# Optimization experiments

Measured on AMD Instinct MI355X. Metric: run time of the kernel, lower is better.

## Reference

```python
import jax, jax.numpy as jnp
import numpy as np

B, T, P, E = 4, 16, 256, 768
H, D = 12, 64          # num_heads, kq_size; H*D == E
DFF = 3072
SCALE = D ** (-0.5)
EPS = 1e-5


def _ln(x, g, b):
    m = jnp.mean(x, axis=-1, keepdims=True)
    v = jnp.mean((x - m) ** 2, axis=-1, keepdims=True)
    return (x - m) / jnp.sqrt(v + EPS) * g + b


def setup_inputs() -> dict:
    key = jax.random.key(0)
    ks = jax.random.split(key, 16)
    std = 0.02
    d = {"x": jax.random.normal(ks[0], (B, T, P, E), jnp.float32)}
    # spatial attention params (weights stored as (in, out))
    d["sq_w"] = jax.random.normal(ks[1], (E, H * D), jnp.float32) * std
    d["sk_w"] = jax.random.normal(ks[2], (E, H * D), jnp.float32) * std
    d["sv_w"] = jax.random.normal(ks[3], (E, H * D), jnp.float32) * std
    d["so_w"] = jax.random.normal(ks[4], (H * D, E), jnp.float32) * std
    d["sq_b"] = jnp.zeros((H * D,), jnp.float32)
    d["sk_b"] = jnp.zeros((H * D,), jnp.float32)
    d["sv_b"] = jnp.zeros((H * D,), jnp.float32)
    d["so_b"] = jnp.zeros((E,), jnp.float32)
    d["sg"] = jnp.ones((E,), jnp.float32)
    d["sb"] = jnp.zeros((E,), jnp.float32)
    # temporal attention params
    d["tq_w"] = jax.random.normal(ks[5], (E, H * D), jnp.float32) * std
    d["tk_w"] = jax.random.normal(ks[6], (E, H * D), jnp.float32) * std
    d["tv_w"] = jax.random.normal(ks[7], (E, H * D), jnp.float32) * std
    d["to_w"] = jax.random.normal(ks[8], (H * D, E), jnp.float32) * std
    d["tq_b"] = jnp.zeros((H * D,), jnp.float32)
    d["tk_b"] = jnp.zeros((H * D,), jnp.float32)
    d["tv_b"] = jnp.zeros((H * D,), jnp.float32)
    d["to_b"] = jnp.zeros((E,), jnp.float32)
    d["tg"] = jnp.ones((E,), jnp.float32)
    d["tb"] = jnp.zeros((E,), jnp.float32)
    # FFN + final layernorm
    d["w1"] = jax.random.normal(ks[9], (E, DFF), jnp.float32) * std
    d["b1"] = jnp.zeros((DFF,), jnp.float32)
    d["w2"] = jax.random.normal(ks[10], (DFF, E), jnp.float32) * std
    d["b2"] = jnp.zeros((E,), jnp.float32)
    d["g"] = jnp.ones((E,), jnp.float32)
    d["bb"] = jnp.zeros((E,), jnp.float32)
    return d


def reference(x, sq_w, sq_b, sk_w, sk_b, sv_w, sv_b, so_w, so_b, sg, sb,
              tq_w, tq_b, tk_w, tk_b, tv_w, tv_b, to_w, to_b, tg, tb,
              w1, b1, w2, b2, g, bb):
    b, t, p, e = x.shape

    # ---- Spatial layer: attention over patches P within each frame ----
    q = (x @ sq_w + sq_b).reshape(b, t, p, H, D)
    k = (x @ sk_w + sk_b).reshape(b, t, p, H, D)
    v = (x @ sv_w + sv_b).reshape(b, t, p, H, D)
    attn = jnp.einsum('btphd,btqhd->bthpq', q, k) * SCALE
    attn = jax.nn.softmax(attn, axis=-1)
    out = jnp.einsum('bthpq,btqhd->btphd', attn, v).reshape(b, t, p, H * D)
    out = out @ so_w + so_b
    x = _ln(x + out, sg, sb)

    # ---- Temporal layer: causal attention over frames T per patch ----
    q = (x @ tq_w + tq_b).reshape(b, t, p, H, D)
    k = (x @ tk_w + tk_b).reshape(b, t, p, H, D)
    v = (x @ tv_w + tv_b).reshape(b, t, p, H, D)
    attn = jnp.einsum('btphd,bsphd->bphts', q, k) * SCALE
    causal = jnp.where(jnp.arange(t)[:, None] >= jnp.arange(t)[None, :],
                       jnp.float32(0), -jnp.inf).astype(x.dtype)  # (T, T)
    attn = attn + causal
    attn = jax.nn.softmax(attn, axis=-1)
    out = jnp.einsum('bphts,bsphd->btphd', attn, v).reshape(b, t, p, H * D)
    out = out @ to_w + to_b
    x = _ln(x + out, tg, tb)

    # ---- Feed forward + final layernorm ----
    ff = jax.nn.gelu(x @ w1 + b1, approximate=False) @ w2 + b2
    x = _ln(x + ff, g, bb)
    return x
```

## Files before the change

### kernel.cpp

```cpp
#include <hip/hip_runtime.h>
#include <math.h>

constexpr int cB   = 4;
constexpr int cT   = 16;
constexpr int cP   = 256;
constexpr int cE   = 768;
constexpr int cH   = 12;
constexpr int cD   = 64;
constexpr int cDFF = 3072;
constexpr int NTOK = cB * cT * cP;
constexpr float cSCALE = 0.125f;
constexpr float cEPS = 1e-5f;

typedef __attribute__((ext_vector_type(8))) short short8;
typedef __attribute__((ext_vector_type(4))) float f32x4;
typedef __attribute__((ext_vector_type(8))) unsigned short u16x8;
typedef __attribute__((ext_vector_type(4))) unsigned short u16x4;

#define AS1 __attribute__((address_space(1)))
#define AS3 __attribute__((address_space(3)))

__device__ inline float b2f(unsigned short u) {
    union { unsigned int i; float f; } c; c.i = ((unsigned int)u) << 16; return c.f;
}
__device__ inline unsigned short f2b(float f) {
    union { float f; unsigned int i; } c; c.f = f;
    unsigned int i = c.i;
    unsigned int r = i + 0x7FFFu + ((i >> 16) & 1u);
    return (unsigned short)(r >> 16);
}

__device__ inline void gload16(const unsigned short* g, short* l) {
    __builtin_amdgcn_global_load_lds((AS1 const void*)g, (AS3 void*)l, 16, 0, 0);
}

template<int OUTB, int ACT, int SPLIT3>
__global__ __launch_bounds__(512, 1) void gemm256_kernel(
    const unsigned short* __restrict__ A,
    const unsigned short* __restrict__ BT,
    const float* __restrict__ bias0, const float* __restrict__ bias1,
    const float* __restrict__ bias2,
    void* __restrict__ C0, void* __restrict__ C1, void* __restrict__ C2,
    int M, int N, int K, int nbn)
{
    __shared__ short LDS[3 * 24576];

    const int tid = threadIdx.x;
    const int w = tid >> 6, l = tid & 63;
    const int l15 = l & 15, l16 = l >> 4;
    const int wm = w >> 1, wn = w & 1;
    const int srow = l >> 3;
    const int sslot = l & 7;

    const int nwg = gridDim.x;
    const int wg = (blockIdx.x & 7) * (nwg >> 3) + (blockIdx.x >> 3);
    const int bm = wg / nbn, bn = wg % nbn;
    const int m0 = bm * 256, n0 = bn * 128;

    f32x4 acc[4][4];
    #pragma unroll
    for (int i = 0; i < 4; ++i)
        #pragma unroll
        for (int j = 0; j < 4; ++j)
            #pragma unroll
            for (int r = 0; r < 4; ++r) acc[i][j][r] = 0.f;

    const int nt = K >> 6;

    const unsigned short* gA[4];
    const unsigned short* gB[2];
    int dA[4], dB[2];
    #pragma unroll
    for (int j = 0; j < 4; ++j) {
        const int r = w * 32 + j * 8 + srow;
        gA[j] = A + (size_t)(m0 + r) * K + ((sslot ^ (r & 7)) << 3);
        dA[j] = r * 64 + (sslot << 3);
    }
    #pragma unroll
    for (int j = 0; j < 2; ++j) {
        const int r = w * 8 + j * 64 + srow;
        gB[j] = BT + (size_t)(n0 + r) * K + ((sslot ^ (r & 7)) << 3);
        dB[j] = 16384 + r * 64 + (sslot << 3);
    }

    int offA[4][2], offB[4][2];
    #pragma unroll
    for (int mm = 0; mm < 4; ++mm) {
        const int ra = wm * 64 + mm * 16 + l15;
        const int sw = (ra & 7) << 4;
        offA[mm][0] = ra * 128 + ((l16 * 16) ^ sw);
        offA[mm][1] = ra * 128 + ((64 + l16 * 16) ^ sw);
    }
    #pragma unroll
    for (int nf = 0; nf < 4; ++nf) {
        const int rb = wn * 64 + nf * 16 + l15;
        const int sw = (rb & 7) << 4;
        offB[nf][0] = 32768 + rb * 128 + ((l16 * 16) ^ sw);
        offB[nf][1] = 32768 + rb * 128 + ((64 + l16 * 16) ^ sw);
    }

    #pragma unroll
    for (int j = 0; j < 4; ++j) { gload16(gA[j], LDS + dA[j]); }
    #pragma unroll
    for (int j = 0; j < 2; ++j) { gload16(gB[j], LDS + dB[j]); }
    #pragma unroll
    for (int j = 0; j < 4; ++j) { gload16(gA[j] + 64, LDS + 24576 + dA[j]); }
    #pragma unroll
    for (int j = 0; j < 2; ++j) { gload16(gB[j] + 64, LDS + 24576 + dB[j]); }
    #pragma unroll
    for (int j = 0; j < 4; ++j) gA[j] += 128;
    #pragma unroll
    for (int j = 0; j < 2; ++j) gB[j] += 128;

    asm volatile("s_waitcnt vmcnt(6)" ::: "memory");
    __builtin_amdgcn_s_barrier();

    int buf = 0;
    for (int t = 0; t < nt; ++t) {
        const char* Lb = (const char*)LDS + buf * 49152;

        short8 aF[4][2], bF[4][2];
        #pragma unroll
        for (int mm = 0; mm < 4; ++mm)
            aF[mm][0] = *(const short8*)(Lb + offA[mm][0]);
        #pragma unroll
        for (int nf = 0; nf < 4; ++nf)
            bF[nf][0] = *(const short8*)(Lb + offB[nf][0]);
        __builtin_amdgcn_sched_barrier(0);
        #pragma unroll
        for (int mm = 0; mm < 4; ++mm)
            aF[mm][1] = *(const short8*)(Lb + offA[mm][1]);
        #pragma unroll
        for (int nf = 0; nf < 4; ++nf)
            bF[nf][1] = *(const short8*)(Lb + offB[nf][1]);

        if (t + 2 < nt) {
            const int b2 = (buf == 0) ? 2 : buf - 1;
            short* dst = LDS + b2 * 24576;
            #pragma unroll
            for (int j = 0; j < 4; ++j) { gload16(gA[j], dst + dA[j]); gA[j] += 64; }
            #pragma unroll
            for (int j = 0; j < 2; ++j) { gload16(gB[j], dst + dB[j]); gB[j] += 64; }
        }

        asm volatile("s_waitcnt lgkmcnt(8)" ::: "memory");
        __builtin_amdgcn_sched_barrier(0);
        __builtin_amdgcn_s_setprio(1);
        #pragma unroll
        for (int nf = 0; nf < 4; ++nf)
            #pragma unroll
            for (int mm = 0; mm < 4; ++mm)
                acc[mm][nf] = __builtin_amdgcn_mfma_f32_16x16x32_bf16(
                    aF[mm][0], bF[nf][0], acc[mm][nf], 0, 0, 0);
        __builtin_amdgcn_s_setprio(0);
        asm volatile("s_waitcnt lgkmcnt(0)" ::: "memory");
        __builtin_amdgcn_sched_barrier(0);
        __builtin_amdgcn_s_setprio(1);
        #pragma unroll
        for (int nf = 0; nf < 4; ++nf)
            #pragma unroll
            for (int mm = 0; mm < 4; ++mm)
                acc[mm][nf] = __builtin_amdgcn_mfma_f32_16x16x32_bf16(
                    aF[mm][1], bF[nf][1], acc[mm][nf], 0, 0, 0);
        __builtin_amdgcn_s_setprio(0);

        if (t + 1 < nt) {
            if (t + 2 < nt)
                asm volatile("s_waitcnt vmcnt(6)" ::: "memory");
            else
                asm volatile("s_waitcnt vmcnt(0)" ::: "memory");
            __builtin_amdgcn_s_barrier();
        }
        buf = (buf == 2) ? 0 : buf + 1;
    }

    #pragma unroll
    for (int mf = 0; mf < 4; ++mf) {
        #pragma unroll
        for (int nf = 0; nf < 4; ++nf) {
            const int ng = n0 + wn * 64 + nf * 16 + l15;
            int nl = ng;
            const float* bp = bias0;
            void* Cp = C0;
            int Nout = N;
            if (SPLIT3) {
                const int which = ng / 768;
                nl = ng - which * 768;
                bp = (which == 0) ? bias0 : (which == 1) ? bias1 : bias2;
                Cp = (which == 0) ? C0 : (which == 1) ? C1 : C2;
                Nout = 768;
            }
            const float bs = bp[nl];
            #pragma unroll
            for (int r = 0; r < 4; ++r) {
                const int row = m0 + wm * 64 + mf * 16 + l16 * 4 + r;
                float v = acc[mf][nf][r] + bs;
                if (ACT) v = 0.5f * v * (1.f + erff(v * 0.70710678118654752f));
                if (OUTB) ((unsigned short*)Cp)[(size_t)row * Nout + nl] = f2b(v);
                else      ((float*)Cp)[(size_t)row * Nout + nl] = v;
            }
        }
    }
}

template<int OUTB, int ACT>
__global__ __launch_bounds__(256) void gemm128_kernel(
    const unsigned short* __restrict__ A,
    const unsigned short* __restrict__ BT,
    const float* __restrict__ bias,
    void* __restrict__ Cout,
    int M, int N, int K)
{
    __shared__ short As[8192];
    __shared__ short Bs[8192];

    const int tid = threadIdx.x;
    const int m0 = blockIdx.y * 128;
    const int n0 = blockIdx.x * 128;
    const int w  = tid >> 6;
    const int l  = tid & 63;
    const int wr = w >> 1, wc = w & 1;
    const int l15 = l & 15, l16 = l >> 4;

    f32x4 acc[4][4];
    #pragma unroll
    for (int i = 0; i < 4; ++i)
        #pragma unroll
        for (int j = 0; j < 4; ++j)
            #pragma unroll
            for (int r = 0; r < 4; ++r) acc[i][j][r] = 0.f;

    const int sr = tid >> 2;
    const int sc = (tid & 3) << 3;
    const unsigned short* ga0 = A  + (size_t)(m0 + sr) * K + sc;
    const unsigned short* ga1 = A  + (size_t)(m0 + 64 + sr) * K + sc;
    const unsigned short* gb0 = BT + (size_t)(n0 + sr) * K + sc;
    const unsigned short* gb1 = BT + (size_t)(n0 + 64 + sr) * K + sc;
    short* lA = As + tid * 8;
    short* lB = Bs + tid * 8;

    const int aoff = (wr * 64 + l15) * 32 + l16 * 8;
    const int boff = (wc * 64 + l15) * 32 + l16 * 8;

    gload16(ga0, lA);
    gload16(ga1, lA + 2048);
    gload16(gb0, lB);
    gload16(gb1, lB + 2048);
    __syncthreads();

    int cur = 0;
    for (int k0 = 0; k0 < K; k0 += 32) {
        if (k0 + 32 < K) {
            const int nb = (cur ^ 1) << 12;
            gload16(ga0 + k0 + 32, lA + nb);
            gload16(ga1 + k0 + 32, lA + nb + 2048);
            gload16(gb0 + k0 + 32, lB + nb);
            gload16(gb1 + k0 + 32, lB + nb + 2048);
        }
        const int cb = cur << 12;
        short8 aF[4], bF[4];
        #pragma unroll
        for (int mf = 0; mf < 4; ++mf)
            aF[mf] = *(const short8*)(As + cb + aoff + mf * 512);
        #pragma unroll
        for (int nf = 0; nf < 4; ++nf)
            bF[nf] = *(const short8*)(Bs + cb + boff + nf * 512);
        #pragma unroll
        for (int mf = 0; mf < 4; ++mf)
            #pragma unroll
            for (int nf = 0; nf < 4; ++nf)
                acc[mf][nf] = __builtin_amdgcn_mfma_f32_16x16x32_bf16(
                    aF[mf], bF[nf], acc[mf][nf], 0, 0, 0);
        __syncthreads();
        cur ^= 1;
    }

    #pragma unroll
    for (int mf = 0; mf < 4; ++mf) {
        #pragma unroll
        for (int nf = 0; nf < 4; ++nf) {
            const int col = n0 + wc * 64 + nf * 16 + l15;
            const float bs = bias[col];
            #pragma unroll
            for (int r = 0; r < 4; ++r) {
                const int row = m0 + wr * 64 + mf * 16 + l16 * 4 + r;
                float v = acc[mf][nf][r] + bs;
                if (ACT) v = 0.5f * v * (1.f + erff(v * 0.70710678118654752f));
                if (OUTB) ((unsigned short*)Cout)[(size_t)row * N + col] = f2b(v);
                else      ((float*)Cout)[(size_t)row * N + col] = v;
            }
        }
    }
}

__global__ __launch_bounds__(256) void transpose_cast_kernel(
    const float* __restrict__ W, unsigned short* __restrict__ WT,
    int K, int N)
{
    __shared__ float t[32][33];
    const int k0 = blockIdx.y * 32;
    const int n0 = blockIdx.x * 32;
    const int tx = threadIdx.x & 31;
    const int ty4 = (threadIdx.x >> 5) << 2;
    #pragma unroll
    for (int i = 0; i < 4; ++i)
        t[ty4 + i][tx] = W[(size_t)(k0 + ty4 + i) * N + n0 + tx];
    __syncthreads();
    #pragma unroll
    for (int i = 0; i < 4; ++i)
        WT[(size_t)(n0 + ty4 + i) * K + k0 + tx] = f2b(t[tx][ty4 + i]);
}

struct TP8 { const float* src[8]; unsigned short* dst[8]; };
__global__ __launch_bounds__(256) void transpose_cast8_kernel(TP8 p)
{
    __shared__ float t[32][33];
    const int z = blockIdx.z;
    const float* W = p.src[z];
    unsigned short* WT = p.dst[z];
    const int k0 = blockIdx.y * 32;
    const int n0 = blockIdx.x * 32;
    const int tx = threadIdx.x & 31;
    const int ty4 = (threadIdx.x >> 5) << 2;
    #pragma unroll
    for (int i = 0; i < 4; ++i)
        t[ty4 + i][tx] = W[(size_t)(k0 + ty4 + i) * cE + n0 + tx];
    __syncthreads();
    #pragma unroll
    for (int i = 0; i < 4; ++i)
        WT[(size_t)(n0 + ty4 + i) * cE + k0 + tx] = f2b(t[tx][ty4 + i]);
}

__global__ __launch_bounds__(256) void cast_bf16_kernel(
    const float* __restrict__ in, unsigned short* __restrict__ out, int n4)
{
    for (int i = blockIdx.x * blockDim.x + threadIdx.x; i < n4;
         i += gridDim.x * blockDim.x) {
        float4 v = ((const float4*)in)[i];
        u16x4 o;
        o[0] = f2b(v.x); o[1] = f2b(v.y); o[2] = f2b(v.z); o[3] = f2b(v.w);
        *(u16x4*)(out + (size_t)i * 4) = o;
    }
}

__global__ __launch_bounds__(256) void residual_ln_kernel(
    const float* __restrict__ X, const unsigned short* __restrict__ R,
    const float* __restrict__ gamma, const float* __restrict__ beta,
    float* __restrict__ out, unsigned short* __restrict__ outb)
{
    const int row = blockIdx.x;
    const size_t off = (size_t)row * cE;
    const int tid = threadIdx.x;

    float v[3];
    float s = 0.f, ss = 0.f;
    #pragma unroll
    for (int i = 0; i < 3; ++i) {
        const int e = tid + i * 256;
        const float t = X[off + e] + b2f(R[off + e]);
        v[i] = t; s += t; ss += t * t;
    }
    #pragma unroll
    for (int o = 32; o > 0; o >>= 1) {
        s  += __shfl_down(s, o);
        ss += __shfl_down(ss, o);
    }
    __shared__ float rs[4], rss[4];
    const int wid = tid >> 6;
    if ((tid & 63) == 0) { rs[wid] = s; rss[wid] = ss; }
    __syncthreads();
    s  = rs[0] + rs[1] + rs[2] + rs[3];
    ss = rss[0] + rss[1] + rss[2] + rss[3];

    const float mean = s * (1.f / cE);
    const float var  = ss * (1.f / cE) - mean * mean;
    const float inv  = rsqrtf(var + cEPS);
    #pragma unroll
    for (int i = 0; i < 3; ++i) {
        const int e = tid + i * 256;
        const float r = (v[i] - mean) * inv * gamma[e] + beta[e];
        out[off + e] = r;
        if (outb) outb[off + e] = f2b(r);
    }
}

__global__ __launch_bounds__(256) void spatial_attn_mfma_kernel(
    const unsigned short* __restrict__ Q, const unsigned short* __restrict__ K,
    const unsigned short* __restrict__ V, unsigned short* __restrict__ O)
{
    __shared__ short Ks[64 * 64];
    __shared__ short Vt[64 * 64];
    __shared__ short Ps[4][64 * 64];

    const int bid = blockIdx.x;
    const int h  = bid % cH;
    const int bt = bid / cH;
    const size_t base = (size_t)bt * cP * cE + h * cD;

    const int tid = threadIdx.x;
    const int w = tid >> 6, l = tid & 63;
    const int l15 = l & 15, l16 = l >> 4;

    short8 qf[4][2];
    #pragma unroll
    for (int mf = 0; mf < 4; ++mf)
        #pragma unroll
        for (int kf = 0; kf < 2; ++kf)
            qf[mf][kf] = *(const short8*)(
                Q + base + (size_t)(w * 64 + mf * 16 + l15) * cE + kf * 32 + l16 * 8);

    f32x4 o[4][4];
    float mrun[4][4], lrun[4][4];
    #pragma unroll
    for (int mf = 0; mf < 4; ++mf)
        #pragma unroll
        for (int j = 0; j < 4; ++j) {
            #pragma unroll
            for (int r = 0; r < 4; ++r) o[mf][j][r] = 0.f;
            mrun[mf][j] = -INFINITY; lrun[mf][j] = 0.f;
        }

    const int krow = w * 8 + (l >> 3);
    const int kc16 = l & 7;
    const int vj  = tid & 31;
    const int vd0 = (tid >> 5) * 8;

    for (int c0 = 0; c0 < cP; c0 += 64) {
        __syncthreads();
        #pragma unroll
        for (int p = 0; p < 2; ++p) {
            const int row = p * 32 + krow;
            gload16(K + base + (size_t)(c0 + row) * cE + ((kc16 ^ (row & 7)) << 3),
                    Ks + row * 64 + kc16 * 8);
        }
        #pragma unroll
        for (int p = 0; p < 2; ++p) {
            const int j = p * 32 + vj;
            short8 vv = *(const short8*)(V + base + (size_t)(c0 + j) * cE + vd0);
            char* vb = (char*)Vt;
            #pragma unroll
            for (int e = 0; e < 8; ++e) {
                const int row = vd0 + e;
                *(short*)(vb + row * 128 + ((2 * j) ^ ((row & 7) << 4))) = vv[e];
            }
        }
        __syncthreads();

        f32x4 s[4][4];
        #pragma unroll
        for (int mf = 0; mf < 4; ++mf)
            #pragma unroll
            for (int nf = 0; nf < 4; ++nf)
                #pragma unroll
                for (int r = 0; r < 4; ++r) s[mf][nf][r] = 0.f;

        #pragma unroll
        for (int nf = 0; nf < 4; ++nf) {
            const int row = nf * 16 + l15;
            const char* kb = (const char*)Ks + row * 128;
            const int sw = (row & 7) << 4;
            short8 k0 = *(const short8*)(kb + ((l16 * 16) ^ sw));
            short8 k1 = *(const short8*)(kb + ((64 + l16 * 16) ^ sw));
            #pragma unroll
            for (int mf = 0; mf < 4; ++mf) {
                s[mf][nf] = __builtin_amdgcn_mfma_f32_16x16x32_bf16(qf[mf][0], k0, s[mf][nf], 0, 0, 0);
                s[mf][nf] = __builtin_amdgcn_mfma_f32_16x16x32_bf16(qf[mf][1], k1, s[mf][nf], 0, 0, 0);
            }
        }

        #pragma unroll
        for (int mf = 0; mf < 4; ++mf)
            #pragma unroll
            for (int nf = 0; nf < 4; ++nf)
                #pragma unroll
                for (int r = 0; r < 4; ++r) s[mf][nf][r] *= cSCALE;

        #pragma unroll
        for (int mf = 0; mf < 4; ++mf) {
            #pragma unroll
            for (int r = 0; r < 4; ++r) {
                float rv = fmaxf(fmaxf(s[mf][0][r], s[mf][1][r]),
                                 fmaxf(s[mf][2][r], s[mf][3][r]));
                rv = fmaxf(rv, __shfl_xor(rv, 1));
                rv = fmaxf(rv, __shfl_xor(rv, 2));
                rv = fmaxf(rv, __shfl_xor(rv, 4));
                rv = fmaxf(rv, __shfl_xor(rv, 8));
                const float mn = fmaxf(mrun[mf][r], rv);
                const float al = __expf(mrun[mf][r] - mn);
                mrun[mf][r] = mn;
                float ps = 0.f;
                #pragma unroll
                for (int nf = 0; nf < 4; ++nf) {
                    const float pe = __expf(s[mf][nf][r] - mn);
                    s[mf][nf][r] = pe;
                    ps += pe;
                }
                ps += __shfl_xor(ps, 1);
                ps += __shfl_xor(ps, 2);
                ps += __shfl_xor(ps, 4);
                ps += __shfl_xor(ps, 8);
                lrun[mf][r] = lrun[mf][r] * al + ps;
                #pragma unroll
                for (int df = 0; df < 4; ++df) o[mf][df][r] *= al;
            }
        }

        char* pw = (char*)&Ps[w][0];
        #pragma unroll
        for (int mf = 0; mf < 4; ++mf)
            #pragma unroll
            for (int nf = 0; nf < 4; ++nf)
                #pragma unroll
                for (int r = 0; r < 4; ++r) {
                    const int row = mf * 16 + l16 * 4 + r;
                    *(short*)(pw + row * 128 + (((nf * 16 + l15) * 2) ^ ((row & 7) << 4))) =
                        (short)f2b(s[mf][nf][r]);
                }

        short8 pa[4][2];
        #pragma unroll
        for (int mf = 0; mf < 4; ++mf) {
            const int prow = mf * 16 + l15;
            const char* pb = (const char*)&Ps[w][0] + prow * 128;
            const int sw = (prow & 7) << 4;
            pa[mf][0] = *(const short8*)(pb + ((l16 * 16) ^ sw));
            pa[mf][1] = *(const short8*)(pb + ((64 + l16 * 16) ^ sw));
        }
        #pragma unroll
        for (int df = 0; df < 4; ++df) {
            const int vrow = df * 16 + l15;
            const char* vbb = (const char*)Vt + vrow * 128;
            const int sw = (vrow & 7) << 4;
            short8 v0 = *(const short8*)(vbb + ((l16 * 16) ^ sw));
            short8 v1 = *(const short8*)(vbb + ((64 + l16 * 16) ^ sw));
            #pragma unroll
            for (int mf = 0; mf < 4; ++mf) {
                o[mf][df] = __builtin_amdgcn_mfma_f32_16x16x32_bf16(pa[mf][0], v0, o[mf][df], 0, 0, 0);
                o[mf][df] = __builtin_amdgcn_mfma_f32_16x16x32_bf16(pa[mf][1], v1, o[mf][df], 0, 0, 0);
            }
        }
    }

    #pragma unroll
    for (int mf = 0; mf < 4; ++mf)
        #pragma unroll
        for (int r = 0; r < 4; ++r) {
            const float inv = 1.f / lrun[mf][r];
            const size_t rowoff = base + (size_t)(w * 64 + mf * 16 + l16 * 4 + r) * cE;
            #pragma unroll
            for (int df = 0; df < 4; ++df)
                O[rowoff + df * 16 + l15] = f2b(o[mf][df][r] * inv);
        }
}

__global__ __launch_bounds__(128) void temporal_attn_kernel(
    const unsigned short* __restrict__ Q, const unsigned short* __restrict__ Kb,
    const unsigned short* __restrict__ V, unsigned short* __restrict__ O)
{
    const int bid = blockIdx.x;
    const int hg  = bid & 1;
    const int bp  = bid >> 1;
    const int p   = bp % cP;
    const int b   = bp / cP;

    __shared__ float Ks[cT][6][cD + 1];
    __shared__ float Vs[cT][6][cD + 1];

    const size_t framestride = (size_t)cP * cE;
    const size_t base0 = ((size_t)(b * cT) * cP + p) * cE + hg * 384;

    for (int li = threadIdx.x; li < cT * 384; li += 128) {
        const int s = li / 384;
        const int r = li % 384;
        const size_t src = base0 + (size_t)s * framestride + r;
        Ks[s][r / 64][r & 63] = b2f(Kb[src]);
        Vs[s][r / 64][r & 63] = b2f(V[src]);
    }
    __syncthreads();
    if (threadIdx.x >= 96) return;

    const int hh = threadIdx.x >> 4;
    const int t  = threadIdx.x & 15;
    const size_t qoff = ((size_t)(b * cT + t) * cP + p) * cE + hg * 384 + hh * cD;

    float q[cD];
    #pragma unroll
    for (int d = 0; d < cD; d += 8) {
        short8 f = *(const short8*)(Q + qoff + d);
        #pragma unroll
        for (int j = 0; j < 8; ++j) q[d + j] = b2f((unsigned short)f[j]);
    }

    float sc[cT];
    float mx = -INFINITY;
    #pragma unroll
    for (int s = 0; s < cT; ++s) {
        float acc = 0.f;
        #pragma unroll
        for (int d = 0; d < cD; ++d) acc = fmaf(q[d], Ks[s][hh][d], acc);
        sc[s] = (s <= t) ? acc * cSCALE : -INFINITY;
        mx = fmaxf(mx, sc[s]);
    }
    float l = 0.f;
    #pragma unroll
    for (int s = 0; s < cT; ++s) {
        const float e_ = __expf(sc[s] - mx);
        sc[s] = e_;
        l += e_;
    }
    float o[cD];
    #pragma unroll
    for (int d = 0; d < cD; ++d) o[d] = 0.f;
    #pragma unroll
    for (int s = 0; s < cT; ++s) {
        const float pj = sc[s];
        #pragma unroll
        for (int d = 0; d < cD; ++d) o[d] = fmaf(pj, Vs[s][hh][d], o[d]);
    }
    const float invl = 1.f / l;
    unsigned short* op = O + qoff;
    #pragma unroll
    for (int d = 0; d < cD; d += 8) {
        u16x8 f;
        #pragma unroll
        for (int j = 0; j < 8; ++j) f[j] = f2b(o[d + j] * invl);
        *(u16x8*)(op + d) = f;
    }
}

extern "C" void kernel_launch(void* const* d_in, const int* in_sizes, int n_in,
                              void* d_out, int out_size, void* d_ws, size_t ws_size,
                              hipStream_t stream)
{
    const float* x    = (const float*)d_in[0];
    const float* sq_w = (const float*)d_in[1];
    const float* sk_w = (const float*)d_in[2];
    const float* sv_w = (const float*)d_in[3];
    const float* so_w = (const float*)d_in[4];
    const float* sq_b = (const float*)d_in[5];
    const float* sk_b = (const float*)d_in[6];
    const float* sv_b = (const float*)d_in[7];
    const float* so_b = (const float*)d_in[8];
    const float* sg   = (const float*)d_in[9];
    const float* sb   = (const float*)d_in[10];
    const float* tq_w = (const float*)d_in[11];
    const float* tk_w = (const float*)d_in[12];
    const float* tv_w = (const float*)d_in[13];
    const float* to_w = (const float*)d_in[14];
    const float* tq_b = (const float*)d_in[15];
    const float* tk_b = (const float*)d_in[16];
    const float* tv_b = (const float*)d_in[17];
    const float* to_b = (const float*)d_in[18];
    const float* tg   = (const float*)d_in[19];
    const float* tb   = (const float*)d_in[20];
    const float* w1   = (const float*)d_in[21];
    const float* b1   = (const float*)d_in[22];
    const float* w2   = (const float*)d_in[23];
    const float* b2   = (const float*)d_in[24];
    const float* g    = (const float*)d_in[25];
    const float* bb   = (const float*)d_in[26];

    const size_t NE = (size_t)NTOK * cE;
    const size_t EE = (size_t)cE * cE;

    float* W0 = (float*)d_ws;
    float* Wp = W0 + NE;
    unsigned short* Rb = (unsigned short*)Wp;
    unsigned short* Xb = (unsigned short*)(Wp + NE);
    unsigned short* Qb = Xb + NE;
    unsigned short* Kbuf = Qb + NE;
    unsigned short* Vb = Kbuf + NE;
    unsigned short* Ob = Vb + NE;
    unsigned short* Hb = Qb;
    unsigned short* WT = Ob + NE;
    unsigned short* sqT = WT;
    unsigned short* skT = sqT + EE;
    unsigned short* svT = skT + EE;
    unsigned short* soT = svT + EE;
    unsigned short* tqT = soT + EE;
    unsigned short* tkT = tqT + EE;
    unsigned short* tvT = tkT + EE;
    unsigned short* toT = tvT + EE;
    unsigned short* w1T = toT + EE;
    unsigned short* w2T = w1T + (size_t)cDFF * cE;

    const dim3 blk(256);
    const dim3 blk512(512);
    const dim3 gLN(NTOK);
    const dim3 gQKV(1152);
    const dim3 gFF1(1536);
    const dim3 g128(cE / 128, NTOK / 128);

    cast_bf16_kernel<<<dim3(2048), blk, 0, stream>>>(x, Xb, (int)(NE / 4));
    {
        TP8 p;
        p.src[0] = sq_w; p.dst[0] = sqT;
        p.src[1] = sk_w; p.dst[1] = skT;
        p.src[2] = sv_w; p.dst[2] = svT;
        p.src[3] = so_w; p.dst[3] = soT;
        p.src[4] = tq_w; p.dst[4] = tqT;
        p.src[5] = tk_w; p.dst[5] = tkT;
        p.src[6] = tv_w; p.dst[6] = tvT;
        p.src[7] = to_w; p.dst[7] = toT;
        transpose_cast8_kernel<<<dim3(cE / 32, cE / 32, 8), blk, 0, stream>>>(p);
    }
    transpose_cast_kernel<<<dim3(cDFF / 32, cE / 32), blk, 0, stream>>>(w1, w1T, cE, cDFF);
    transpose_cast_kernel<<<dim3(cE / 32, cDFF / 32), blk, 0, stream>>>(w2, w2T, cDFF, cE);

    gemm256_kernel<1,0,1><<<gQKV, blk512, 0, stream>>>(
        Xb, sqT, sq_b, sk_b, sv_b, Qb, Kbuf, Vb, NTOK, 2304, cE, 18);
    spatial_attn_mfma_kernel<<<dim3(cB * cT * cH), blk, 0, stream>>>(Qb, Kbuf, Vb, Ob);
    gemm128_kernel<1,0><<<g128, blk, 0, stream>>>(Ob, soT, so_b, Rb, NTOK, cE, cE);
    residual_ln_kernel<<<gLN, blk, 0, stream>>>(x, Rb, sg, sb, W0, Xb);

    gemm256_kernel<1,0,1><<<gQKV, blk512, 0, stream>>>(
        Xb, tqT, tq_b, tk_b, tv_b, Qb, Kbuf, Vb, NTOK, 2304, cE, 18);
    temporal_attn_kernel<<<dim3(cB * cP * 2), dim3(128), 0, stream>>>(Qb, Kbuf, Vb, Ob);
    gemm128_kernel<1,0><<<g128, blk, 0, stream>>>(Ob, toT, to_b, Rb, NTOK, cE, cE);
    residual_ln_kernel<<<gLN, blk, 0, stream>>>(W0, Rb, tg, tb, W0, Xb);

    gemm256_kernel<1,1,0><<<gFF1, blk512, 0, stream>>>(
        Xb, w1T, b1, nullptr, nullptr, Hb, nullptr, nullptr, NTOK, cDFF, cE, 24);
    gemm128_kernel<1,0><<<g128, blk, 0, stream>>>(Hb, w2T, b2, Rb, NTOK, cE, cDFF);
    residual_ln_kernel<<<gLN, blk, 0, stream>>>(W0, Rb, g, bb, (float*)d_out, nullptr);
}
```

Measured before the change: 711.2 us.

## Make 256x128 GEMM persistent with contiguous tile ranges and cross-tile prefetch

Converts the 256x128 bf16 GEMM into a persistent kernel launched with 256 workgroups, one per CU. Each workgroup walks a contiguous range of output tiles, and the global-to-LDS prefetch pipeline continues across tile boundaries, with the epilogue running inline as each tile finishes. The aim is to cut per-workgroup launch and prologue cost and to keep the load pipeline from draining between tiles. It adds loop-control overhead and a barrier at every tile boundary. The A/B reuse pattern also changes, since consecutive tiles on one CU now share the same A rows rather than being spread by the old swizzle.

```diff
diff --git a/kernel.cpp b/kernel.cpp
--- a/kernel.cpp
+++ b/kernel.cpp
@@ -35,13 +35,13 @@
 }
 
 template<int OUTB, int ACT, int SPLIT3>
-__global__ __launch_bounds__(512, 1) void gemm256_kernel(
+__global__ __launch_bounds__(512, 1) void gemm256p_kernel(
     const unsigned short* __restrict__ A,
     const unsigned short* __restrict__ BT,
     const float* __restrict__ bias0, const float* __restrict__ bias1,
     const float* __restrict__ bias2,
     void* __restrict__ C0, void* __restrict__ C1, void* __restrict__ C2,
-    int M, int N, int K, int nbn)
+    int M, int N, int K, int nbn, int ntiles)
 {
     __shared__ short LDS[3 * 24576];
 
@@ -52,10 +52,14 @@
     const int srow = l >> 3;
     const int sslot = l & 7;
 
-    const int nwg = gridDim.x;
-    const int wg = (blockIdx.x & 7) * (nwg >> 3) + (blockIdx.x >> 3);
-    const int bm = wg / nbn, bn = wg % nbn;
-    const int m0 = bm * 256, n0 = bn * 128;
+    const int nblk = gridDim.x;
+    const int blk = (blockIdx.x & 7) * (nblk >> 3) + (blockIdx.x >> 3);
+    const int q = ntiles / nblk, r = ntiles % nblk;
+    const int t0 = blk * q + (blk < r ? blk : r);
+    const int tcount = q + (blk < r ? 1 : 0);
+    const int nt = K >> 6;
+    const int total = tcount * nt;
+    if (total == 0) return;
 
     f32x4 acc[4][4];
     #pragma unroll
@@ -63,24 +67,21 @@
         #pragma unroll
         for (int j = 0; j < 4; ++j)
             #pragma unroll
-            for (int r = 0; r < 4; ++r) acc[i][j][r] = 0.f;
-
-    const int nt = K >> 6;
-
-    const unsigned short* gA[4];
-    const unsigned short* gB[2];
-    int dA[4], dB[2];
+            for (int rr = 0; rr < 4; ++rr) acc[i][j][rr] = 0.f;
+
+    size_t laneA[4]; int dAo[4];
     #pragma unroll
     for (int j = 0; j < 4; ++j) {
-        const int r = w * 32 + j * 8 + srow;
-        gA[j] = A + (size_t)(m0 + r) * K + ((sslot ^ (r & 7)) << 3);
-        dA[j] = r * 64 + (sslot << 3);
-    }
+        const int rr = w * 32 + j * 8 + srow;
+        laneA[j] = (size_t)rr * K + ((sslot ^ (rr & 7)) << 3);
+        dAo[j] = rr * 64 + (sslot << 3);
+    }
+    size_t laneB[2]; int dBo[2];
     #pragma unroll
     for (int j = 0; j < 2; ++j) {
-        const int r = w * 8 + j * 64 + srow;
-        gB[j] = BT + (size_t)(n0 + r) * K + ((sslot ^ (r & 7)) << 3);
-        dB[j] = 16384 + r * 64 + (sslot << 3);
+        const int rr = w * 8 + j * 64 + srow;
+        laneB[j] = (size_t)rr * K + ((sslot ^ (rr & 7)) << 3);
+        dBo[j] = 16384 + rr * 64 + (sslot << 3);
     }
 
     int offA[4][2], offB[4][2];
@@ -99,25 +100,37 @@
         offB[nf][1] = 32768 + rb * 128 + ((64 + l16 * 16) ^ sw);
     }
 
-    #pragma unroll
-    for (int j = 0; j < 4; ++j) { gload16(gA[j], LDS + dA[j]); }
-    #pragma unroll
-    for (int j = 0; j < 2; ++j) { gload16(gB[j], LDS + dB[j]); }
-    #pragma unroll
-    for (int j = 0; j < 4; ++j) { gload16(gA[j] + 64, LDS + 24576 + dA[j]); }
-    #pragma unroll
-    for (int j = 0; j < 2; ++j) { gload16(gB[j] + 64, LDS + 24576 + dB[j]); }
-    #pragma unroll
-    for (int j = 0; j < 4; ++j) gA[j] += 128;
-    #pragma unroll
-    for (int j = 0; j < 2; ++j) gB[j] += 128;
-
+    int s_bm = t0 / nbn, s_bn = t0 % nbn, s_kt = 0;
+    size_t sAb = (size_t)s_bm * 256 * K;
+    size_t sBb = (size_t)s_bn * 128 * K;
+
+    #define STAGE(buf_)                                                       \
+        {                                                                     \
+            const unsigned short* a_ = A + sAb + s_kt * 64;                   \
+            const unsigned short* b_ = BT + sBb + s_kt * 64;                  \
+            short* d_ = LDS + (buf_) * 24576;                                 \
+            _Pragma("unroll")                                                 \
+            for (int j_ = 0; j_ < 4; ++j_) gload16(a_ + laneA[j_], d_ + dAo[j_]); \
+            _Pragma("unroll")                                                 \
+            for (int j_ = 0; j_ < 2; ++j_) gload16(b_ + laneB[j_], d_ + dBo[j_]); \
+            if (++s_kt == nt) {                                               \
+                s_kt = 0;                                                     \
+                if (++s_bn == nbn) { s_bn = 0; sBb = 0; sAb += (size_t)256 * K; } \
+                else sBb += (size_t)128 * K;                                  \
+            }                                                                 \
+        }
+
+    STAGE(0);
+    STAGE(1);
     asm volatile("s_waitcnt vmcnt(6)" ::: "memory");
     __builtin_amdgcn_s_barrier();
 
+    int cbm = t0 / nbn, cbn = t0 % nbn, ckt = 0;
     int buf = 0;
-    for (int t = 0; t < nt; ++t) {
+
+    for (int g = 0; g < total; ++g) {
         const char* Lb = (const char*)LDS + buf * 49152;
+        const bool boundary = (ckt == nt - 1);
 
         short8 aF[4][2], bF[4][2];
         #pragma unroll
@@ -134,13 +147,9 @@
         for (int nf = 0; nf < 4; ++nf)
             bF[nf][1] = *(const short8*)(Lb + offB[nf][1]);
 
-        if (t + 2 < nt) {
+        if (!boundary && g + 2 < total) {
             const int b2 = (buf == 0) ? 2 : buf - 1;
-            short* dst = LDS + b2 * 24576;
-            #pragma unroll
-            for (int j = 0; j < 4; ++j) { gload16(gA[j], dst + dA[j]); gA[j] += 64; }
-            #pragma unroll
-            for (int j = 0; j < 2; ++j) { gload16(gB[j], dst + dB[j]); gB[j] += 64; }
+            STAGE(b2);
         }
 
         asm volatile("s_waitcnt lgkmcnt(8)" ::: "memory");
@@ -164,43 +173,60 @@
                     aF[mm][1], bF[nf][1], acc[mm][nf], 0, 0, 0);
         __builtin_amdgcn_s_setprio(0);
 
-        if (t + 1 < nt) {
-            if (t + 2 < nt)
+        if (boundary) {
+            const int m0 = cbm * 256;
+            const int n0c = cbn * 128;
+            #pragma unroll
+            for (int mf = 0; mf < 4; ++mf) {
+                #pragma unroll
+                for (int nf = 0; nf < 4; ++nf) {
+                    const int ng = n0c + wn * 64 + nf * 16 + l15;
+                    int nl = ng;
+                    const float* bp = bias0;
+                    void* Cp = C0;
+                    int Nout = N;
+                    if (SPLIT3) {
+                        const int which = ng / 768;
+                        nl = ng - which * 768;
+                        bp = (which == 0) ? bias0 : (which == 1) ? bias1 : bias2;
+                        Cp = (which == 0) ? C0 : (which == 1) ? C1 : C2;
+                        Nout = 768;
+                    }
+                    const float bs = bp[nl];
+                    #pragma unroll
+                    for (int rr = 0; rr < 4; ++rr) {
+                        const int row = m0 + wm * 64 + mf * 16 + l16 * 4 + rr;
+                        float v = acc[mf][nf][rr] + bs;
+                        if (ACT) v = 0.5f * v * (1.f + erff(v * 0.70710678118654752f));
+                        if (OUTB) ((unsigned short*)Cp)[(size_t)row * Nout + nl] = f2b(v);
+                        else      ((float*)Cp)[(size_t)row * Nout + nl] = v;
+                        acc[mf][nf][rr] = 0.f;
+                    }
+                }
+            }
+            if (g + 1 < total) {
                 asm volatile("s_waitcnt vmcnt(6)" ::: "memory");
-            else
-                asm volatile("s_waitcnt vmcnt(0)" ::: "memory");
-            __builtin_amdgcn_s_barrier();
+                __builtin_amdgcn_s_barrier();
+                if (g + 2 < total) {
+                    const int b2 = (buf == 0) ? 2 : buf - 1;
+                    STAGE(b2);
+                }
+            }
+            ckt = 0;
+            if (++cbn == nbn) { cbn = 0; ++cbm; }
+        } else {
+            if (g + 1 < total) {
+                if (g + 2 < total)
+                    asm volatile("s_waitcnt vmcnt(6)" ::: "memory");
+                else
+                    asm volatile("s_waitcnt vmcnt(0)" ::: "memory");
+                __builtin_amdgcn_s_barrier();
+            }
+            ++ckt;
         }
         buf = (buf == 2) ? 0 : buf + 1;
     }
-
-    #pragma unroll
-    for (int mf = 0; mf < 4; ++mf) {
-        #pragma unroll
-        for (int nf = 0; nf < 4; ++nf) {
-            const int ng = n0 + wn * 64 + nf * 16 + l15;
-            int nl = ng;
-            const float* bp = bias0;
-            void* Cp = C0;
-            int Nout = N;
-            if (SPLIT3) {
-                const int which = ng / 768;
-                nl = ng - which * 768;
-                bp = (which == 0) ? bias0 : (which == 1) ? bias1 : bias2;
-                Cp = (which == 0) ? C0 : (which == 1) ? C1 : C2;
-                Nout = 768;
-            }
-            const float bs = bp[nl];
-            #pragma unroll
-            for (int r = 0; r < 4; ++r) {
-                const int row = m0 + wm * 64 + mf * 16 + l16 * 4 + r;
-                float v = acc[mf][nf][r] + bs;
-                if (ACT) v = 0.5f * v * (1.f + erff(v * 0.70710678118654752f));
-                if (OUTB) ((unsigned short*)Cp)[(size_t)row * Nout + nl] = f2b(v);
-                else      ((float*)Cp)[(size_t)row * Nout + nl] = v;
-            }
-        }
-    }
+    #undef STAGE
 }
 
 template<int OUTB, int ACT>
@@ -687,8 +713,7 @@
     const dim3 blk(256);
     const dim3 blk512(512);
     const dim3 gLN(NTOK);
-    const dim3 gQKV(1152);
-    const dim3 gFF1(1536);
+    const dim3 gP(256);
     const dim3 g128(cE / 128, NTOK / 128);
 
     cast_bf16_kernel<<<dim3(2048), blk, 0, stream>>>(x, Xb, (int)(NE / 4));
@@ -707,20 +732,20 @@
     transpose_cast_kernel<<<dim3(cDFF / 32, cE / 32), blk, 0, stream>>>(w1, w1T, cE, cDFF);
     transpose_cast_kernel<<<dim3(cE / 32, cDFF / 32), blk, 0, stream>>>(w2, w2T, cDFF, cE);
 
-    gemm256_kernel<1,0,1><<<gQKV, blk512, 0, stream>>>(
-        Xb, sqT, sq_b, sk_b, sv_b, Qb, Kbuf, Vb, NTOK, 2304, cE, 18);
+    gemm256p_kernel<1,0,1><<<gP, blk512, 0, stream>>>(
+        Xb, sqT, sq_b, sk_b, sv_b, Qb, Kbuf, Vb, NTOK, 2304, cE, 18, 1152);
     spatial_attn_mfma_kernel<<<dim3(cB * cT * cH), blk, 0, stream>>>(Qb, Kbuf, Vb, Ob);
     gemm128_kernel<1,0><<<g128, blk, 0, stream>>>(Ob, soT, so_b, Rb, NTOK, cE, cE);
     residual_ln_kernel<<<gLN, blk, 0, stream>>>(x, Rb, sg, sb, W0, Xb);
 
-    gemm256_kernel<1,0,1><<<gQKV, blk512, 0, stream>>>(
-        Xb, tqT, tq_b, tk_b, tv_b, Qb, Kbuf, Vb, NTOK, 2304, cE, 18);
+    gemm256p_kernel<1,0,1><<<gP, blk512, 0, stream>>>(
+        Xb, tqT, tq_b, tk_b, tv_b, Qb, Kbuf, Vb, NTOK, 2304, cE, 18, 1152);
     temporal_attn_kernel<<<dim3(cB * cP * 2), dim3(128), 0, stream>>>(Qb, Kbuf, Vb, Ob);
     gemm128_kernel<1,0><<<g128, blk, 0, stream>>>(Ob, toT, to_b, Rb, NTOK, cE, cE);
     residual_ln_kernel<<<gLN, blk, 0, stream>>>(W0, Rb, tg, tb, W0, Xb);
 
-    gemm256_kernel<1,1,0><<<gFF1, blk512, 0, stream>>>(
-        Xb, w1T, b1, nullptr, nullptr, Hb, nullptr, nullptr, NTOK, cDFF, cE, 24);
+    gemm256p_kernel<1,1,0><<<gP, blk512, 0, stream>>>(
+        Xb, w1T, b1, nullptr, nullptr, Hb, nullptr, nullptr, NTOK, cDFF, cE, 24, 1536);
     gemm128_kernel<1,0><<<g128, blk, 0, stream>>>(Hb, w2T, b2, Rb, NTOK, cE, cDFF);
     residual_ln_kernel<<<gLN, blk, 0, stream>>>(W0, Rb, g, bb, (float*)d_out, nullptr);
 }
```

Result: no change. 705.5 us (-0.8%).

## Widen QKV/FF1 GEMM tile to 256x256 with double-buffered LDS

Applied to the files above, without the earlier changes.

The wide GEMM now computes 256x256 output tiles instead of 256x128, with eight waves arranged 2x4 and each wave holding 8x4 MFMA accumulators. The LDS pipeline moves from three 48KB stages with two tiles in flight to two 64KB buffers with one prefetch in flight and a full vmcnt(0) wait each iteration. The aim is more operand reuse per byte loaded and fewer workgroups. The cost is higher register pressure, less latency hiding, and half as many workgroups (576 and 768) to spread across the CUs.

```diff
diff --git a/kernel.cpp b/kernel.cpp
--- a/kernel.cpp
+++ b/kernel.cpp
@@ -35,7 +35,7 @@
 }
 
 template<int OUTB, int ACT, int SPLIT3>
-__global__ __launch_bounds__(512, 1) void gemm256_kernel(
+__global__ __launch_bounds__(512, 1) void gemm256w_kernel(
     const unsigned short* __restrict__ A,
     const unsigned short* __restrict__ BT,
     const float* __restrict__ bias0, const float* __restrict__ bias1,
@@ -43,23 +43,26 @@
     void* __restrict__ C0, void* __restrict__ C1, void* __restrict__ C2,
     int M, int N, int K, int nbn)
 {
-    __shared__ short LDS[3 * 24576];
+    __shared__ short LDS[2 * 32768];
 
     const int tid = threadIdx.x;
     const int w = tid >> 6, l = tid & 63;
     const int l15 = l & 15, l16 = l >> 4;
-    const int wm = w >> 1, wn = w & 1;
-    const int srow = l >> 3;
-    const int sslot = l & 7;
+    const int wm = w >> 2, wn = w & 3;
+    const int strow = tid >> 3;
+    const int stslot = tid & 7;
 
     const int nwg = gridDim.x;
     const int wg = (blockIdx.x & 7) * (nwg >> 3) + (blockIdx.x >> 3);
     const int bm = wg / nbn, bn = wg % nbn;
-    const int m0 = bm * 256, n0 = bn * 128;
-
-    f32x4 acc[4][4];
-    #pragma unroll
-    for (int i = 0; i < 4; ++i)
+    const int m0 = bm * 256, n0 = bn * 256;
+
+    const unsigned short* pA = A + (size_t)m0 * K;
+    const unsigned short* pB = BT + (size_t)n0 * K;
+
+    f32x4 acc[8][4];
+    #pragma unroll
+    for (int i = 0; i < 8; ++i)
         #pragma unroll
         for (int j = 0; j < 4; ++j)
             #pragma unroll
@@ -67,26 +70,30 @@
 
     const int nt = K >> 6;
 
-    const unsigned short* gA[4];
-    const unsigned short* gB[2];
-    int dA[4], dB[2];
+    size_t laneS[4]; int dS[4];
     #pragma unroll
     for (int j = 0; j < 4; ++j) {
-        const int r = w * 32 + j * 8 + srow;
-        gA[j] = A + (size_t)(m0 + r) * K + ((sslot ^ (r & 7)) << 3);
-        dA[j] = r * 64 + (sslot << 3);
-    }
-    #pragma unroll
-    for (int j = 0; j < 2; ++j) {
-        const int r = w * 8 + j * 64 + srow;
-        gB[j] = BT + (size_t)(n0 + r) * K + ((sslot ^ (r & 7)) << 3);
-        dB[j] = 16384 + r * 64 + (sslot << 3);
-    }
-
-    int offA[4][2], offB[4][2];
-    #pragma unroll
-    for (int mm = 0; mm < 4; ++mm) {
-        const int ra = wm * 64 + mm * 16 + l15;
+        const int row = j * 64 + strow;
+        laneS[j] = (size_t)row * K + ((stslot ^ (row & 7)) << 3);
+        dS[j] = row * 64 + (stslot << 3);
+    }
+
+    #define STAGE(buf_, kt_)                                                  \
+        {                                                                     \
+            const unsigned short* a_ = pA + (kt_) * 64;                       \
+            const unsigned short* b_ = pB + (kt_) * 64;                       \
+            short* d_ = LDS + (buf_) * 32768;                                 \
+            _Pragma("unroll")                                                 \
+            for (int j_ = 0; j_ < 4; ++j_) {                                  \
+                gload16(a_ + laneS[j_], d_ + dS[j_]);                         \
+                gload16(b_ + laneS[j_], d_ + 16384 + dS[j_]);                 \
+            }                                                                 \
+        }
+
+    int offA[8][2], offB[4][2];
+    #pragma unroll
+    for (int mm = 0; mm < 8; ++mm) {
+        const int ra = wm * 128 + mm * 16 + l15;
         const int sw = (ra & 7) << 4;
         offA[mm][0] = ra * 128 + ((l16 * 16) ^ sw);
         offA[mm][1] = ra * 128 + ((64 + l16 * 16) ^ sw);
@@ -99,57 +106,37 @@
         offB[nf][1] = 32768 + rb * 128 + ((64 + l16 * 16) ^ sw);
     }
 
-    #pragma unroll
-    for (int j = 0; j < 4; ++j) { gload16(gA[j], LDS + dA[j]); }
-    #pragma unroll
-    for (int j = 0; j < 2; ++j) { gload16(gB[j], LDS + dB[j]); }
-    #pragma unroll
-    for (int j = 0; j < 4; ++j) { gload16(gA[j] + 64, LDS + 24576 + dA[j]); }
-    #pragma unroll
-    for (int j = 0; j < 2; ++j) { gload16(gB[j] + 64, LDS + 24576 + dB[j]); }
-    #pragma unroll
-    for (int j = 0; j < 4; ++j) gA[j] += 128;
-    #pragma unroll
-    for (int j = 0; j < 2; ++j) gB[j] += 128;
-
-    asm volatile("s_waitcnt vmcnt(6)" ::: "memory");
+    STAGE(0, 0);
+    asm volatile("s_waitcnt vmcnt(0)" ::: "memory");
     __builtin_amdgcn_s_barrier();
 
     int buf = 0;
     for (int t = 0; t < nt; ++t) {
-        const char* Lb = (const char*)LDS + buf * 49152;
-
-        short8 aF[4][2], bF[4][2];
-        #pragma unroll
-        for (int mm = 0; mm < 4; ++mm)
+        if (t + 1 < nt) STAGE(buf ^ 1, t + 1);
+
+        const char* Lb = (const char*)LDS + buf * 65536;
+        short8 aF[8][2], bF[4][2];
+        #pragma unroll
+        for (int mm = 0; mm < 8; ++mm)
             aF[mm][0] = *(const short8*)(Lb + offA[mm][0]);
         #pragma unroll
         for (int nf = 0; nf < 4; ++nf)
             bF[nf][0] = *(const short8*)(Lb + offB[nf][0]);
         __builtin_amdgcn_sched_barrier(0);
         #pragma unroll
-        for (int mm = 0; mm < 4; ++mm)
+        for (int mm = 0; mm < 8; ++mm)
             aF[mm][1] = *(const short8*)(Lb + offA[mm][1]);
         #pragma unroll
         for (int nf = 0; nf < 4; ++nf)
             bF[nf][1] = *(const short8*)(Lb + offB[nf][1]);
 
-        if (t + 2 < nt) {
-            const int b2 = (buf == 0) ? 2 : buf - 1;
-            short* dst = LDS + b2 * 24576;
-            #pragma unroll
-            for (int j = 0; j < 4; ++j) { gload16(gA[j], dst + dA[j]); gA[j] += 64; }
-            #pragma unroll
-            for (int j = 0; j < 2; ++j) { gload16(gB[j], dst + dB[j]); gB[j] += 64; }
-        }
-
-        asm volatile("s_waitcnt lgkmcnt(8)" ::: "memory");
+        asm volatile("s_waitcnt lgkmcnt(12)" ::: "memory");
         __builtin_amdgcn_sched_barrier(0);
         __builtin_amdgcn_s_setprio(1);
         #pragma unroll
         for (int nf = 0; nf < 4; ++nf)
             #pragma unroll
-            for (int mm = 0; mm < 4; ++mm)
+            for (int mm = 0; mm < 8; ++mm)
                 acc[mm][nf] = __builtin_amdgcn_mfma_f32_16x16x32_bf16(
                     aF[mm][0], bF[nf][0], acc[mm][nf], 0, 0, 0);
         __builtin_amdgcn_s_setprio(0);
@@ -159,23 +146,21 @@
         #pragma unroll
         for (int nf = 0; nf < 4; ++nf)
             #pragma unroll
-            for (int mm = 0; mm < 4; ++mm)
+            for (int mm = 0; mm < 8; ++mm)
                 acc[mm][nf] = __builtin_amdgcn_mfma_f32_16x16x32_bf16(
                     aF[mm][1], bF[nf][1], acc[mm][nf], 0, 0, 0);
         __builtin_amdgcn_s_setprio(0);
 
         if (t + 1 < nt) {
-            if (t + 2 < nt)
-                asm volatile("s_waitcnt vmcnt(6)" ::: "memory");
-            else
-                asm volatile("s_waitcnt vmcnt(0)" ::: "memory");
+            asm volatile("s_waitcnt vmcnt(0)" ::: "memory");
             __builtin_amdgcn_s_barrier();
         }
-        buf = (buf == 2) ? 0 : buf + 1;
-    }
-
-    #pragma unroll
-    for (int mf = 0; mf < 4; ++mf) {
+        buf ^= 1;
+    }
+    #undef STAGE
+
+    #pragma unroll
+    for (int mf = 0; mf < 8; ++mf) {
         #pragma unroll
         for (int nf = 0; nf < 4; ++nf) {
             const int ng = n0 + wn * 64 + nf * 16 + l15;
@@ -193,7 +178,7 @@
             const float bs = bp[nl];
             #pragma unroll
             for (int r = 0; r < 4; ++r) {
-                const int row = m0 + wm * 64 + mf * 16 + l16 * 4 + r;
+                const int row = m0 + wm * 128 + mf * 16 + l16 * 4 + r;
                 float v = acc[mf][nf][r] + bs;
                 if (ACT) v = 0.5f * v * (1.f + erff(v * 0.70710678118654752f));
                 if (OUTB) ((unsigned short*)Cp)[(size_t)row * Nout + nl] = f2b(v);
@@ -383,6 +368,7 @@
         if (outb) outb[off + e] = f2b(r);
     }
 }
+
 
 __global__ __launch_bounds__(256) void spatial_attn_mfma_kernel(
     const unsigned short* __restrict__ Q, const unsigned short* __restrict__ K,
@@ -687,8 +673,8 @@
     const dim3 blk(256);
     const dim3 blk512(512);
     const dim3 gLN(NTOK);
-    const dim3 gQKV(1152);
-    const dim3 gFF1(1536);
+    const dim3 gQKV(576);
+    const dim3 gFF1(768);
     const dim3 g128(cE / 128, NTOK / 128);
 
     cast_bf16_kernel<<<dim3(2048), blk, 0, stream>>>(x, Xb, (int)(NE / 4));
@@ -707,20 +693,20 @@
     transpose_cast_kernel<<<dim3(cDFF / 32, cE / 32), blk, 0, stream>>>(w1, w1T, cE, cDFF);
     transpose_cast_kernel<<<dim3(cE / 32, cDFF / 32), blk, 0, stream>>>(w2, w2T, cDFF, cE);
 
-    gemm256_kernel<1,0,1><<<gQKV, blk512, 0, stream>>>(
-        Xb, sqT, sq_b, sk_b, sv_b, Qb, Kbuf, Vb, NTOK, 2304, cE, 18);
+    gemm256w_kernel<1,0,1><<<gQKV, blk512, 0, stream>>>(
+        Xb, sqT, sq_b, sk_b, sv_b, Qb, Kbuf, Vb, NTOK, 2304, cE, 9);
     spatial_attn_mfma_kernel<<<dim3(cB * cT * cH), blk, 0, stream>>>(Qb, Kbuf, Vb, Ob);
     gemm128_kernel<1,0><<<g128, blk, 0, stream>>>(Ob, soT, so_b, Rb, NTOK, cE, cE);
     residual_ln_kernel<<<gLN, blk, 0, stream>>>(x, Rb, sg, sb, W0, Xb);
 
-    gemm256_kernel<1,0,1><<<gQKV, blk512, 0, stream>>>(
-        Xb, tqT, tq_b, tk_b, tv_b, Qb, Kbuf, Vb, NTOK, 2304, cE, 18);
+    gemm256w_kernel<1,0,1><<<gQKV, blk512, 0, stream>>>(
+        Xb, tqT, tq_b, tk_b, tv_b, Qb, Kbuf, Vb, NTOK, 2304, cE, 9);
     temporal_attn_kernel<<<dim3(cB * cP * 2), dim3(128), 0, stream>>>(Qb, Kbuf, Vb, Ob);
     gemm128_kernel<1,0><<<g128, blk, 0, stream>>>(Ob, toT, to_b, Rb, NTOK, cE, cE);
     residual_ln_kernel<<<gLN, blk, 0, stream>>>(W0, Rb, tg, tb, W0, Xb);
 
-    gemm256_kernel<1,1,0><<<gFF1, blk512, 0, stream>>>(
-        Xb, w1T, b1, nullptr, nullptr, Hb, nullptr, nullptr, NTOK, cDFF, cE, 24);
+    gemm256w_kernel<1,1,0><<<gFF1, blk512, 0, stream>>>(
+        Xb, w1T, b1, nullptr, nullptr, Hb, nullptr, nullptr, NTOK, cDFF, cE, 12);
     gemm128_kernel<1,0><<<g128, blk, 0, stream>>>(Hb, w2T, b2, Rb, NTOK, cE, cDFF);
     residual_ln_kernel<<<gLN, blk, 0, stream>>>(W0, Rb, g, bb, (float*)d_out, nullptr);
 }
```

Measured after the change: 704.1 us. No clear change (-1.0%).
